# Kernel optimization log

Measured on AMD Instinct MI355X. Metric: run time of the kernel, lower is better.

The kernel has to match this reference:

```python
import jax, jax.numpy as jnp
import numpy as np

KERNEL = 11  # matches AttnBlock(kernel_size=11)
EPS = 1e-4


def _patches(x, k):
    """Extract k x k patches (stride 1, VALID), matching nn.Unfold ordering.

    x: [B, C, H, W] -> ([B, L, C*k*k], (Hp, Wp)) with L = Hp*Wp.
    """
    p = jax.lax.conv_general_dilated_patches(x, (k, k), (1, 1), 'VALID')  # [B, C*k*k, Hp, Wp]
    B, D, Hp, Wp = p.shape
    return p.reshape(B, D, Hp * Wp).transpose(0, 2, 1), (Hp, Wp)


def setup_inputs() -> dict:
    key = jax.random.key(0)
    k1, k2 = jax.random.split(key)
    im1 = jax.random.normal(k1, (4, 64, 40, 40), dtype=jnp.float32)
    im2 = jax.random.normal(k2, (4, 64, 40, 40), dtype=jnp.float32)
    return {"im1": im1, "im2": im2}


def reference(im1, im2):
    k = KERNEL
    # Dynamic per-sample filters from im1 patches, L2-normalized per patch.
    p1, _ = _patches(im1, k)                                  # [B, L, D], D = C*k*k
    norm = jnp.sqrt(jnp.sum(p1 * p1, axis=-1, keepdims=True))  # [B, L, 1]
    p1n = p1 / jnp.maximum(norm, EPS)
    # conv2d(im2, filters) with stride 1 / no padding == dot of im2 patches with filters.
    p2, (Hp, Wp) = _patches(im2, k)                           # [B, P, D], P = Hp*Wp
    scores = jnp.einsum('bld,bpd->bpl', p1n, p2)              # [B, P, L]
    out = jnp.max(scores, axis=-1)                            # max over filter (channel) dim
    B = im1.shape[0]
    return out.reshape(B, 1, Hp, Wp)
```

## Files before the change

### kernel.cpp

```cpp
#include <hip/hip_runtime.h>

#define C_    64
#define H_    40
#define W_    40
#define KS    11
#define HP    30
#define NB    4
#define NL    900
#define ND    59
#define EPSF  1e-4f
#define PCH   6
#define PCHB  10
#define NCHB  3
#define SCW   65
#define SCB   33
#define NINF  -3.4e38f
#define MPAD  1664
#define GBLK  1600
#define GBATCH (1600 * 1600)
#define GSTEPT 65600

typedef _Float16 f16x8 __attribute__((ext_vector_type(8)));
typedef float    f32x4 __attribute__((ext_vector_type(4)));

__global__ __launch_bounds__(128)
void k_pack(const float* __restrict__ im2, const float* __restrict__ im1,
            _Float16* __restrict__ packed, float* __restrict__ ssqbuf,
            unsigned int* __restrict__ keys) {
    const int blk = blockIdx.x, b = blockIdx.y, img = blockIdx.z;
    const int pos = blk * 128 + threadIdx.x;
    const float* src = (img ? im1 : im2) + b * C_ * 1600;
    _Float16* dst = packed + ((size_t)img * NB + b) * (8 * MPAD * 8);
    float ss = 0.f;
    #pragma unroll
    for (int oct = 0; oct < 8; ++oct) {
        f16x8 h = {};
        if (pos < 1600) {
            #pragma unroll
            for (int j = 0; j < 8; ++j) {
                float v = src[(oct * 8 + j) * 1600 + pos];
                h[j] = (_Float16)v;
                ss += v * v;
            }
        }
        *(f16x8*)&dst[(oct * MPAD + pos) * 8] = h;
    }
    if (img == 1 && pos < 1600) ssqbuf[b * 1600 + pos] = ss;
    if (img == 0 && pos < NL) keys[b * NL + pos] = 0u;
}

__global__ __launch_bounds__(256, 3)
void k_gram(const _Float16* __restrict__ packed, _Float16* __restrict__ G,
            const float* __restrict__ ssqbuf, float* __restrict__ invnorm) {
    const int i = blockIdx.x, j = blockIdx.y, b = blockIdx.z;
    const int tid = threadIdx.x;
    __shared__ __align__(16) _Float16 smem[128 * 136];

    int dd = i - j; if (dd < 0) dd = -dd;
    if (dd > 10) {
        if (i < j) {
            const int part = (j == 11) ? 0 : ((i == 0) ? 1 : 2);
            const int ly0 = part * 10;
            float* ssq = (float*)smem;
            float* colsum = ssq + 800;
            for (int t = tid; t < 800; t += 256)
                ssq[t] = ssqbuf[b * 1600 + ly0 * W_ + t];
            __syncthreads();
            for (int t = tid; t < 10 * W_; t += 256) {
                int yy = t / W_, x = t - yy * W_;
                float s = 0.f;
                #pragma unroll
                for (int r = 0; r < KS; ++r) s += ssq[(yy + r) * W_ + x];
                colsum[t] = s;
            }
            __syncthreads();
            for (int t = tid; t < 10 * HP; t += 256) {
                int ly = t / HP, lx = t - ly * HP;
                float s = 0.f;
                #pragma unroll
                for (int sx = 0; sx < KS; ++sx) s += colsum[ly * W_ + lx + sx];
                invnorm[b * NL + (ly0 + ly) * HP + lx] = 1.f / fmaxf(sqrtf(s), EPSF);
            }
        }
        return;
    }
    const int w = tid >> 6, L = tid & 63, lq = L >> 4, lr = L & 15;

    _Float16 (*As)[128][8] = (_Float16 (*)[128][8])smem;
    _Float16 (*Bs)[128][8] = (_Float16 (*)[128][8])(smem + 8192);

    const _Float16* pa = packed + (size_t)b * (8 * MPAD * 8);
    const _Float16* pb = packed + (size_t)(NB + b) * (8 * MPAD * 8);
    for (int t = tid; t < 1024; t += 256) {
        int oct = t >> 7, m = t & 127;
        *(f16x8*)&As[oct][m][0] = *(const f16x8*)&pa[(oct * MPAD + i * 128 + m) * 8];
        *(f16x8*)&Bs[oct][m][0] = *(const f16x8*)&pb[(oct * MPAD + j * 128 + m) * 8];
    }
    __syncthreads();

    const int mb = (w & 1) * 64, nb = (w >> 1) * 64;
    f16x8 a0[4], a1[4], b0[4], b1[4];
    #pragma unroll
    for (int q = 0; q < 4; ++q) {
        a0[q] = *(const f16x8*)&As[lq][mb + q * 16 + lr][0];
        a1[q] = *(const f16x8*)&As[4 + lq][mb + q * 16 + lr][0];
        b0[q] = *(const f16x8*)&Bs[lq][nb + q * 16 + lr][0];
        b1[q] = *(const f16x8*)&Bs[4 + lq][nb + q * 16 + lr][0];
    }
    f32x4 acc[4][4];
    #pragma unroll
    for (int mi = 0; mi < 4; ++mi)
        #pragma unroll
        for (int ni = 0; ni < 4; ++ni) {
            f32x4 c = {0.f, 0.f, 0.f, 0.f};
            c = __builtin_amdgcn_mfma_f32_16x16x32_f16(a0[mi], b0[ni], c, 0, 0, 0);
            c = __builtin_amdgcn_mfma_f32_16x16x32_f16(a1[mi], b1[ni], c, 0, 0, 0);
            acc[mi][ni] = c;
        }
    __syncthreads();
    #pragma unroll
    for (int mi = 0; mi < 4; ++mi)
        #pragma unroll
        for (int ni = 0; ni < 4; ++ni)
            #pragma unroll
            for (int rg = 0; rg < 4; ++rg)
                smem[(mb + mi * 16 + lq * 4 + rg) * 136 + nb + ni * 16 + lr] =
                    (_Float16)acc[mi][ni][rg];
    __syncthreads();
    _Float16* Gb = G + (size_t)b * GBATCH;
    for (int t = tid; t < 2048; t += 256) {
        int row = t >> 4, seg = t & 15;
        int m = i * 128 + row, n = j * 128 + seg * 8;
        if (m < 1600 && n < 1600) {
            int r = m / 40, mr = m - r * 40;
            int c = n / 40, nc = n - c * 40;
            *(f16x8*)&Gb[(size_t)(r * 40 + c) * GBLK + mr * 40 + nc] =
                *(const f16x8*)&smem[row * 136 + seg * 8];
        }
    }
}

__global__ __launch_bounds__(256, 4)
void k_box(const _Float16* __restrict__ G, const float* __restrict__ invnorm,
           unsigned int* __restrict__ keys) {
    __shared__ float csum[1600];
    __shared__ float scratch[HP * SCB];
    __shared__ float sInv[PCHB * HP];
    const int chunk = blockIdx.x;
    const int dy = (int)blockIdx.y - (HP - 1);
    const int b = blockIdx.z;
    const int ady = dy < 0 ? -dy : dy;
    const int rows = HP - ady;
    if (chunk * PCHB >= rows) return;
    const int pyLo = dy < 0 ? -dy : 0;
    const int py0 = pyLo + chunk * PCHB;
    const int P = min(PCHB, rows - chunk * PCHB);
    const int tid = threadIdx.x;

    for (int t = tid; t < P * HP; t += 256) {
        int i = t / HP, lx = t - i * HP;
        sInv[i * HP + lx] = invnorm[b * NL + (py0 + i + dy) * HP + lx];
    }

    const _Float16* Gb = G + (size_t)b * GBATCH;
    float s[8];
    f16x8 qa, qs;
    const _Float16* base = nullptr;
    if (tid < 200) {
        base = Gb + (size_t)(py0 * 41 + dy) * GBLK + tid * 8;
        #pragma unroll
        for (int j = 0; j < 8; ++j) s[j] = 0.f;
        for (int r = 0; r < KS; ++r) {
            f16x8 q = *(const f16x8*)(base + r * GSTEPT);
            #pragma unroll
            for (int j = 0; j < 8; ++j) s[j] += (float)q[j];
        }
    }

    for (int i = 0; i < P; ++i) {
        const int py = py0 + i;
        if (tid < 200) {
            if (i > 0) {
                #pragma unroll
                for (int j = 0; j < 8; ++j) s[j] += (float)qa[j] - (float)qs[j];
            }
            float4* c4 = (float4*)(csum + tid * 8);
            c4[0] = make_float4(s[0], s[1], s[2], s[3]);
            c4[1] = make_float4(s[4], s[5], s[6], s[7]);
            if (i + 1 < P) {
                qa = *(const f16x8*)(base + (i + 11) * GSTEPT);
                qs = *(const f16x8*)(base + i * GSTEPT);
            }
        }
        __syncthreads();
        if (tid < 4 * ND) {
            int pg = tid / ND, dxI = tid - ND * pg;
            int dx = dxI - (HP - 1);
            int pxb = (pg < 2) ? (pg << 3) : (16 + (pg - 2) * 7);
            int usz = (pg < 2) ? 8 : 7;
            int u0 = max(0, -dx - pxb), u1 = min(usz - 1, (HP - 1) - dx - pxb);
            if (u0 <= u1) {
                const float* cp = csum + dx;
                float run = 0.f;
                #pragma unroll
                for (int sr = 0; sr < KS; ++sr) run += cp[(pxb + u0 + sr) * (W_ + 1)];
                int u = u0;
                for (;;) {
                    int px = pxb + u;
                    scratch[px * SCB + px + dx] = run;
                    if (++u > u1) break;
                    run += cp[(pxb + u + 10) * (W_ + 1)] - cp[(pxb + u - 1) * (W_ + 1)];
                }
            }
        }
        __syncthreads();
        if (tid < 240) {
            int px = tid >> 3, l = tid & 7;
            const float* srow = scratch + px * SCB;
            const float* inv = sInv + i * HP;
            float m = NINF;
            #pragma unroll
            for (int k = 0; k < 4; ++k) {
                int lx = l + 8 * k;
                if (lx < HP) m = fmaxf(m, srow[lx] * inv[lx]);
            }
            m = fmaxf(m, __shfl_xor(m, 1));
            m = fmaxf(m, __shfl_xor(m, 2));
            m = fmaxf(m, __shfl_xor(m, 4));
            if (l == 0) {
                unsigned int ub = __float_as_uint(m);
                unsigned int k = (ub & 0x80000000u) ? ~ub : (ub | 0x80000000u);
                atomicMax(&keys[b * NL + py * HP + px], k);
            }
        }
    }
}

__global__ __launch_bounds__(256)
void k_decode(const unsigned int* __restrict__ keys, float* __restrict__ out) {
    int i = blockIdx.x * 256 + threadIdx.x;
    if (i < NB * NL) {
        unsigned int k = keys[i];
        unsigned int u = (k & 0x80000000u) ? (k ^ 0x80000000u) : ~k;
        out[i] = __uint_as_float(u);
    }
}

__global__ __launch_bounds__(256)
void k_norm_fb(const float* __restrict__ im1, float* __restrict__ invnorm) {
    const int ly = blockIdx.x, b = blockIdx.y;
    const int tid = threadIdx.x;
    __shared__ float colsq[KS * W_];
    __shared__ float colsum[W_];
    const float* base = im1 + b * C_ * H_ * W_;
    for (int i = tid; i < KS * W_; i += 256) {
        int r = i / W_, x = i - r * W_;
        const float* p = base + (ly + r) * W_ + x;
        float s = 0.f;
        #pragma unroll 8
        for (int c = 0; c < C_; ++c) { float v = p[c * H_ * W_]; s += v * v; }
        colsq[i] = s;
    }
    __syncthreads();
    if (tid < W_) {
        float s = 0.f;
        #pragma unroll
        for (int r = 0; r < KS; ++r) s += colsq[r * W_ + tid];
        colsum[tid] = s;
    }
    __syncthreads();
    if (tid < HP) {
        float s = 0.f;
        #pragma unroll
        for (int sx = 0; sx < KS; ++sx) s += colsum[tid + sx];
        invnorm[b * NL + ly * HP + tid] = 1.f / fmaxf(sqrtf(s), EPSF);
    }
}

#define MAXPL 16
__global__ __launch_bounds__(256, 2)
void k_main_fb(const float* __restrict__ im1, const float* __restrict__ im2,
               const float* __restrict__ invnorm, unsigned int* __restrict__ keys) {
    const int chunk = blockIdx.x;
    const int dy = (int)blockIdx.y - (HP - 1);
    const int b = blockIdx.z;
    const int ady = dy < 0 ? -dy : dy;
    const int rows = HP - ady;
    if (chunk * PCH >= rows) return;
    const int pyLo = dy < 0 ? -dy : 0;
    const int py0 = pyLo + chunk * PCH;
    const int P = min(PCH, rows - chunk * PCH);
    const int nPl = P + KS - 1;
    const int tid = threadIdx.x;
    const int w = tid >> 6, L = tid & 63, lq = L >> 4, lr = L & 15;

    __shared__ __align__(16) _Float16 planes[MAXPL][H_ * W_];
    __shared__ __align__(16) float csum[H_ * W_];
    __shared__ __align__(16) _Float16 Astg[8][48][8];
    __shared__ __align__(16) _Float16 Bstg[8][48][8];
    __shared__ float scratch[HP * SCW];
    __shared__ float partials[120];
    __shared__ float sInv[HP];

    const float* im1b = im1 + b * C_ * H_ * W_;
    const float* im2b = im2 + b * C_ * H_ * W_;
    if (tid < 128) {
        int arr = tid >> 6, r = tid & 63;
        int oct = r >> 3, x = 40 + (r & 7);
        f16x8 z = {};
        *(f16x8*)((arr ? Bstg : Astg)[oct][x]) = z;
    }
    for (int p = 0; p < nPl; ++p) {
        const int y = py0 + p;
        for (int t = tid; t < 640; t += 256) {
            int arr = t >= 320;
            int r = arr ? t - 320 : t;
            int oct = r / 40, x = r - oct * 40;
            const float* pc = (arr ? (im1b + (y + dy) * W_) : (im2b + y * W_))
                              + oct * 8 * H_ * W_ + x;
            f16x8 h;
            #pragma unroll
            for (int j = 0; j < 8; ++j) h[j] = (_Float16)pc[j * H_ * W_];
            *(f16x8*)((arr ? Bstg : Astg)[oct][x]) = h;
        }
        __syncthreads();
        for (int t = w; t < 9; t += 4) {
            int mt = t / 3, nt = t - 3 * mt;
            f16x8 a0 = *(const f16x8*)(Astg[lq][mt * 16 + lr]);
            f16x8 b0 = *(const f16x8*)(Bstg[lq][nt * 16 + lr]);
            f16x8 a1 = *(const f16x8*)(Astg[4 + lq][mt * 16 + lr]);
            f16x8 b1 = *(const f16x8*)(Bstg[4 + lq][nt * 16 + lr]);
            f32x4 acc = {0.f, 0.f, 0.f, 0.f};
            acc = __builtin_amdgcn_mfma_f32_16x16x32_f16(a0, b0, acc, 0, 0, 0);
            acc = __builtin_amdgcn_mfma_f32_16x16x32_f16(a1, b1, acc, 0, 0, 0);
            int x1 = nt * 16 + lr;
            if (x1 < W_) {
                int x2b = mt * 16 + lq * 4;
                #pragma unroll
                for (int rg = 0; rg < 4; ++rg) {
                    int x2 = x2b + rg;
                    if (x2 < W_) planes[p][x2 * W_ + x1] = (_Float16)acc[rg];
                }
            }
        }
        __syncthreads();
    }
    for (int i = 0; i < P; ++i) {
        const int py = py0 + i, ly = py + dy;
        if (tid < 200) {
            float4* c4 = (float4*)(csum + tid * 8);
            if (i == 0) {
                float s[8] = {0.f,0.f,0.f,0.f,0.f,0.f,0.f,0.f};
                #pragma unroll
                for (int r = 0; r < KS; ++r) {
                    f16x8 q = *(const f16x8*)(planes[r] + tid * 8);
                    #pragma unroll
                    for (int j = 0; j < 8; ++j) s[j] += (float)q[j];
                }
                c4[0] = make_float4(s[0], s[1], s[2], s[3]);
                c4[1] = make_float4(s[4], s[5], s[6], s[7]);
            } else {
                f16x8 qa = *(const f16x8*)(planes[i + 10] + tid * 8);
                f16x8 qs = *(const f16x8*)(planes[i - 1] + tid * 8);
                float4 v0 = c4[0], v1 = c4[1];
                v0.x += (float)qa[0] - (float)qs[0]; v0.y += (float)qa[1] - (float)qs[1];
                v0.z += (float)qa[2] - (float)qs[2]; v0.w += (float)qa[3] - (float)qs[3];
                v1.x += (float)qa[4] - (float)qs[4]; v1.y += (float)qa[5] - (float)qs[5];
                v1.z += (float)qa[6] - (float)qs[6]; v1.w += (float)qa[7] - (float)qs[7];
                c4[0] = v0; c4[1] = v1;
            }
        } else if (tid >= 224 && tid < 224 + HP) {
            sInv[tid - 224] = invnorm[b * NL + ly * HP + (tid - 224)];
        }
        __syncthreads();
        for (int t = tid; t < 5 * ND; t += 256) {
            int pg = t / ND, dxI = t - ND * pg;
            int dx = dxI - (HP - 1), pxb = 6 * pg;
            #pragma unroll
            for (int u = 0; u < 6; ++u) scratch[(pxb + u) * SCW + dxI] = NINF;
            int u0 = max(0, -dx - pxb), u1 = min(5, (HP - 1) - dx - pxb);
            if (u0 <= u1) {
                const float* cp = csum + dx;
                float run = 0.f;
                #pragma unroll
                for (int sr = 0; sr < KS; ++sr) run += cp[(pxb + u0 + sr) * (W_ + 1)];
                int u = u0;
                for (;;) {
                    scratch[(pxb + u) * SCW + dxI] = run * sInv[pxb + u + dx];
                    if (++u > u1) break;
                    run += cp[(pxb + u + 10) * (W_ + 1)] - cp[(pxb + u - 1) * (W_ + 1)];
                }
            }
        }
        __syncthreads();
        if (tid < 120) {
            int px = tid >> 2, q = tid & 3;
            float m = NINF;
            int d0 = q * 15, d1 = min(d0 + 15, ND);
            for (int d = d0; d < d1; ++d) m = fmaxf(m, scratch[px * SCW + d]);
            partials[tid] = m;
        }
        __syncthreads();
        if (tid < HP) {
            float m = fmaxf(fmaxf(partials[tid * 4], partials[tid * 4 + 1]),
                            fmaxf(partials[tid * 4 + 2], partials[tid * 4 + 3]));
            unsigned int ub = __float_as_uint(m);
            unsigned int k = (ub & 0x80000000u) ? ~ub : (ub | 0x80000000u);
            atomicMax(&keys[b * NL + py * HP + tid], k);
        }
        __syncthreads();
    }
}

extern "C" void kernel_launch(void* const* d_in, const int* in_sizes, int n_in,
                              void* d_out, int out_size, void* d_ws, size_t ws_size,
                              hipStream_t stream) {
    const float* im1 = (const float*)d_in[0];
    const float* im2 = (const float*)d_in[1];
    unsigned int* keys = (unsigned int*)d_ws;
    float* invnorm = (float*)((char*)d_ws + 14400);
    float* ssqbuf  = (float*)((char*)d_ws + 28800);
    const size_t packedOff = 65536;
    const size_t packedBytes = (size_t)2 * NB * 8 * MPAD * 8 * 2;
    const size_t gOff = packedOff + packedBytes;
    const size_t gBytes = (size_t)NB * GBATCH * 2;
    const size_t needed = gOff + gBytes;

    if (ws_size >= needed) {
        _Float16* packed = (_Float16*)((char*)d_ws + packedOff);
        _Float16* G = (_Float16*)((char*)d_ws + gOff);
        k_pack<<<dim3(13, NB, 2), 128, 0, stream>>>(im2, im1, packed, ssqbuf, keys);
        k_gram<<<dim3(13, 13, NB), 256, 0, stream>>>(packed, G, ssqbuf, invnorm);
        k_box<<<dim3(NCHB, ND, NB), 256, 0, stream>>>(G, invnorm, keys);
    } else {
        hipMemsetAsync(d_ws, 0, NB * NL * sizeof(unsigned int), stream);
        k_norm_fb<<<dim3(HP, NB), 256, 0, stream>>>(im1, invnorm);
        k_main_fb<<<dim3(5, ND, NB), 256, 0, stream>>>(im1, im2, invnorm, keys);
    }
    k_decode<<<(NB * NL + 255) / 256, 256, 0, stream>>>(keys, (float*)d_out);
}
```

Before: 93.93 us.

## Stage G planes in LDS and fuse diagonal box sum into max pass

The box-sum kernel now bulk-loads all needed G planes for its chunk into shared memory up front instead of streaming them from global memory per row. The separate diagonal running-sum pass and its scratch buffer are removed. Each max thread instead computes its 11-term diagonal sum directly from a double-buffered column-sum array, which also drops one barrier per row. This raises LDS use (occupancy hint lowered from 4 to 2 blocks per CU) and replaces the sliding-window sum with a direct 11-term sum per output.

```diff
diff --git a/kernel.cpp b/kernel.cpp
--- a/kernel.cpp
+++ b/kernel.cpp
@@ -12,8 +12,8 @@
 #define PCH   6
 #define PCHB  10
 #define NCHB  3
+#define NPLMAX (PCHB + KS - 1)
 #define SCW   65
-#define SCB   33
 #define NINF  -3.4e38f
 #define MPAD  1664
 #define GBLK  1600
@@ -140,11 +140,11 @@
     }
 }
 
-__global__ __launch_bounds__(256, 4)
+__global__ __launch_bounds__(256, 2)
 void k_box(const _Float16* __restrict__ G, const float* __restrict__ invnorm,
            unsigned int* __restrict__ keys) {
-    __shared__ float csum[1600];
-    __shared__ float scratch[HP * SCB];
+    __shared__ __align__(16) _Float16 pl_lds[NPLMAX * GBLK];
+    __shared__ float csum2[2 * 1600];
     __shared__ float sInv[PCHB * HP];
     const int chunk = blockIdx.x;
     const int dy = (int)blockIdx.y - (HP - 1);
@@ -155,82 +155,68 @@
     const int pyLo = dy < 0 ? -dy : 0;
     const int py0 = pyLo + chunk * PCHB;
     const int P = min(PCHB, rows - chunk * PCHB);
+    const int nPl = P + KS - 1;
     const int tid = threadIdx.x;
 
+    const _Float16* Gb = G + (size_t)b * GBATCH + (size_t)(py0 * 41 + dy) * GBLK;
+    for (int t = tid; t < nPl * 200; t += 256) {
+        int pl = t / 200, e = t - pl * 200;
+        *(f16x8*)&pl_lds[pl * GBLK + e * 8] = *(const f16x8*)&Gb[pl * GSTEPT + e * 8];
+    }
     for (int t = tid; t < P * HP; t += 256) {
         int i = t / HP, lx = t - i * HP;
         sInv[i * HP + lx] = invnorm[b * NL + (py0 + i + dy) * HP + lx];
     }
-
-    const _Float16* Gb = G + (size_t)b * GBATCH;
+    __syncthreads();
+
     float s[8];
-    f16x8 qa, qs;
-    const _Float16* base = nullptr;
     if (tid < 200) {
-        base = Gb + (size_t)(py0 * 41 + dy) * GBLK + tid * 8;
         #pragma unroll
         for (int j = 0; j < 8; ++j) s[j] = 0.f;
         for (int r = 0; r < KS; ++r) {
-            f16x8 q = *(const f16x8*)(base + r * GSTEPT);
+            f16x8 q = *(const f16x8*)&pl_lds[r * GBLK + tid * 8];
             #pragma unroll
             for (int j = 0; j < 8; ++j) s[j] += (float)q[j];
         }
     }
 
     for (int i = 0; i < P; ++i) {
-        const int py = py0 + i;
+        float* cb = csum2 + (i & 1) * 1600;
         if (tid < 200) {
             if (i > 0) {
+                f16x8 qa = *(const f16x8*)&pl_lds[(i + 10) * GBLK + tid * 8];
+                f16x8 qs = *(const f16x8*)&pl_lds[(i - 1) * GBLK + tid * 8];
                 #pragma unroll
                 for (int j = 0; j < 8; ++j) s[j] += (float)qa[j] - (float)qs[j];
             }
-            float4* c4 = (float4*)(csum + tid * 8);
+            float4* c4 = (float4*)(cb + tid * 8);
             c4[0] = make_float4(s[0], s[1], s[2], s[3]);
             c4[1] = make_float4(s[4], s[5], s[6], s[7]);
-            if (i + 1 < P) {
-                qa = *(const f16x8*)(base + (i + 11) * GSTEPT);
-                qs = *(const f16x8*)(base + i * GSTEPT);
-            }
-        }
-        __syncthreads();
-        if (tid < 4 * ND) {
-            int pg = tid / ND, dxI = tid - ND * pg;
-            int dx = dxI - (HP - 1);
-            int pxb = (pg < 2) ? (pg << 3) : (16 + (pg - 2) * 7);
-            int usz = (pg < 2) ? 8 : 7;
-            int u0 = max(0, -dx - pxb), u1 = min(usz - 1, (HP - 1) - dx - pxb);
-            if (u0 <= u1) {
-                const float* cp = csum + dx;
-                float run = 0.f;
-                #pragma unroll
-                for (int sr = 0; sr < KS; ++sr) run += cp[(pxb + u0 + sr) * (W_ + 1)];
-                int u = u0;
-                for (;;) {
-                    int px = pxb + u;
-                    scratch[px * SCB + px + dx] = run;
-                    if (++u > u1) break;
-                    run += cp[(pxb + u + 10) * (W_ + 1)] - cp[(pxb + u - 1) * (W_ + 1)];
-                }
-            }
         }
         __syncthreads();
         if (tid < 240) {
             int px = tid >> 3, l = tid & 7;
-            const float* srow = scratch + px * SCB;
+            const float* cp = cb + px * 40;
             const float* inv = sInv + i * HP;
             float m = NINF;
             #pragma unroll
             for (int k = 0; k < 4; ++k) {
                 int lx = l + 8 * k;
-                if (lx < HP) m = fmaxf(m, srow[lx] * inv[lx]);
+                if (lx < HP) {
+                    const float* cpl = cp + lx;
+                    float run = 0.f;
+                    #pragma unroll
+                    for (int sr = 0; sr < KS; ++sr) run += cpl[sr * 41];
+                    m = fmaxf(m, run * inv[lx]);
+                }
             }
             m = fmaxf(m, __shfl_xor(m, 1));
             m = fmaxf(m, __shfl_xor(m, 2));
             m = fmaxf(m, __shfl_xor(m, 4));
             if (l == 0) {
                 unsigned int ub = __float_as_uint(m);
-                unsigned int k = (ub & 0x80000000u) ? ~ub : (ub | 0x80000000u);
-                atomicMax(&keys[b * NL + py * HP + px], k);
+                unsigned int k2 = (ub & 0x80000000u) ? ~ub : (ub | 0x80000000u);
+                atomicMax(&keys[b * NL + (py0 + i) * HP + px], k2);
             }
         }
     }
```

Result: no change. 92.52 us (median of 2 runs) (-1.5%).
